# Optimization experiments

Measured on AMD Instinct MI355X. Metric: run time of the kernel, lower is better.

The kernel has to match this reference:

```python
import jax, jax.numpy as jnp
import numpy as np

NA = 100000  # number of a-type nodes (rows of adj)
NB = 100000  # number of b-type nodes (cols of adj)
NE = 1600000 # number of edges (nnz of adj)
BF = 128     # b_features
AF = 128     # a_features


def setup_inputs() -> dict:
    key = jax.random.key(0)
    k1, k2, k3, k4, k5, k6 = jax.random.split(key, 6)
    stdv = 1.0 / np.sqrt(BF)
    return {
        "b_input": jax.random.normal(k1, (NB, BF), dtype=jnp.float32),
        "edge_rows": jax.random.randint(k2, (NE,), 0, NA, dtype=jnp.int32),
        "edge_cols": jax.random.randint(k3, (NE,), 0, NB, dtype=jnp.int32),
        "edge_vals": jax.random.uniform(k4, (NE,), dtype=jnp.float32),
        "a_weight": jax.random.uniform(k5, (BF, AF), minval=-stdv, maxval=stdv, dtype=jnp.float32),
        "a_bias": jax.random.uniform(k6, (AF,), minval=-stdv, maxval=stdv, dtype=jnp.float32),
    }


def reference(b_input, edge_rows, edge_cols, edge_vals, a_weight, a_bias):
    # a_support = b_input @ a_weight            : [NB, AF]
    a_support = jnp.matmul(b_input, a_weight)
    # a_output = spmm(adj, a_support)           : [NA, AF]
    # adj[r, c] = edge_vals at (edge_rows, edge_cols)
    gathered = a_support[edge_cols] * edge_vals[:, None]   # [NE, AF]
    a_output = jax.ops.segment_sum(gathered, edge_rows, num_segments=NA)
    # bias=True -> early return of a-side output
    return a_output + a_bias
```

## Files before the change

kernel.cpp:

```cpp
#include <hip/hip_runtime.h>
#include <hip/hip_bf16.h>

#define AF 128
#define BF 128
#define BROWS 64
#define CAP 1600
#define PASSA_CHUNK 8192
#define NBUCK_MAX 1600

typedef __attribute__((ext_vector_type(8))) short bf16x8;
typedef __attribute__((ext_vector_type(4))) float f32x4;

__device__ inline unsigned short f2bf(float f) {
    unsigned int u = __float_as_uint(f);
    u += 0x7FFF + ((u >> 16) & 1);
    return (unsigned short)(u >> 16);
}
__device__ inline unsigned int pk2bf(float x, float y) {
    __hip_bfloat162 h = __float22bfloat162_rn(make_float2(x, y));
    return *(unsigned int*)&h;
}
__device__ inline float bflo(unsigned int u) { return __uint_as_float(u << 16); }
__device__ inline float bfhi(unsigned int u) { return __uint_as_float(u & 0xFFFF0000u); }

__global__ void wtrans_kernel(const float* __restrict__ W, unsigned short* __restrict__ Wt) {
    int idx = blockIdx.x * 256 + threadIdx.x;
    int n = idx & 127, k = idx >> 7;
    Wt[n * 128 + k] = f2bf(W[(size_t)k * 128 + n]);
}

__global__ __launch_bounds__(256) void gemm_mfma_kernel(const float* __restrict__ Bin,
                                                        const unsigned short* __restrict__ Wt,
                                                        unsigned short* __restrict__ Sup, int NB) {
    __shared__ unsigned short As[64][136];
    __shared__ unsigned short Ws[128][136];
    const int tid = threadIdx.x;
    const int lane = tid & 63;
    const int wave = tid >> 6;
    const int row0 = blockIdx.x * 64;

    {
        int lr = tid >> 2;
        int ks = (tid & 3) * 32;
        int gr = row0 + lr;
        const float4* src = (const float4*)(Bin + (size_t)gr * BF + ks);
        #pragma unroll
        for (int i = 0; i < 4; i++) {
            float4 a = (gr < NB) ? src[2 * i]     : make_float4(0.f, 0.f, 0.f, 0.f);
            float4 b = (gr < NB) ? src[2 * i + 1] : make_float4(0.f, 0.f, 0.f, 0.f);
            uint4 u;
            u.x = pk2bf(a.x, a.y); u.y = pk2bf(a.z, a.w);
            u.z = pk2bf(b.x, b.y); u.w = pk2bf(b.z, b.w);
            *(uint4*)(&As[lr][ks + i * 8]) = u;
        }
    }
    {
        int r = tid >> 1;
        int c = (tid & 1) * 64;
        const uint4* src = (const uint4*)(Wt + r * 128 + c);
        uint4* dst = (uint4*)(&Ws[r][c]);
        #pragma unroll
        for (int i = 0; i < 8; i++) dst[i] = src[i];
    }
    __syncthreads();

    const int m = lane & 15;
    const int quad = lane >> 4;

    bf16x8 af[4];
    #pragma unroll
    for (int ks = 0; ks < 4; ks++)
        af[ks] = *(const bf16x8*)(&As[wave * 16 + m][ks * 32 + quad * 8]);

    #pragma unroll
    for (int nt = 0; nt < 8; nt++) {
        f32x4 acc = {0.f, 0.f, 0.f, 0.f};
        #pragma unroll
        for (int ks = 0; ks < 4; ks++) {
            bf16x8 bf = *(const bf16x8*)(&Ws[nt * 16 + m][ks * 32 + quad * 8]);
            acc = __builtin_amdgcn_mfma_f32_16x16x32_bf16(af[ks], bf, acc, 0, 0, 0);
        }
        int f = nt * 16 + m;
        int si = ((f & 63) << 1) | (f >> 6);
        #pragma unroll
        for (int r = 0; r < 4; r++) {
            int row = row0 + wave * 16 + quad * 4 + r;
            if (row < NB) Sup[(size_t)row * AF + si] = f2bf(acc[r]);
        }
    }
}

__global__ __launch_bounds__(256) void passA_kernel(const int* __restrict__ rows,
                                                    const int* __restrict__ cols,
                                                    const float* __restrict__ vals,
                                                    int* __restrict__ grel,
                                                    int2* __restrict__ binned, int NE, int NBUCK) {
    __shared__ int h[NBUCK_MAX];
    __shared__ int rbase[NBUCK_MAX];
    int tid = threadIdx.x;
    for (int i = tid; i < NBUCK; i += 256) h[i] = 0;
    __syncthreads();
    int base = blockIdx.x * PASSA_CHUNK;
    #pragma unroll
    for (int i = 0; i < PASSA_CHUNK / 256; i++) {
        int e = base + tid + i * 256;
        if (e < NE) atomicAdd(&h[rows[e] >> 6], 1);
    }
    __syncthreads();
    for (int k = tid; k < NBUCK; k += 256) {
        int c = h[k];
        rbase[k] = k * CAP + (c ? atomicAdd(&grel[k], c) : 0);
        h[k] = 0;
    }
    __syncthreads();
    #pragma unroll
    for (int i = 0; i < PASSA_CHUNK / 256; i++) {
        int e = base + tid + i * 256;
        if (e < NE) {
            int r = rows[e];
            int k = r >> 6;
            int lp = atomicAdd(&h[k], 1);
            int2 p;
            p.x = cols[e] | ((r & 63) << 17);
            p.y = __float_as_int(vals[e]);
            binned[rbase[k] + lp] = p;
        }
    }
}

__global__ __launch_bounds__(512) void spmm_sorted_kernel(const unsigned short* __restrict__ Sup,
                                                          const int2* __restrict__ binned,
                                                          const int* __restrict__ grel,
                                                          const float* __restrict__ bias,
                                                          float* __restrict__ out, int NA) {
    __shared__ int   spx[CAP];
    __shared__ float spy[CAP];
    __shared__ int cnt[BROWS];
    __shared__ int sc[BROWS];
    __shared__ int rs[BROWS + 1];
    __shared__ int cur[BROWS];
    const int tid = threadIdx.x;
    const int b = blockIdx.x;
    int n = grel[b]; if (n > CAP) n = CAP;
    const int2* src = binned + (size_t)b * CAP;

    int2 pr[4];
    #pragma unroll
    for (int j = 0; j < 4; j++) {
        int i = tid + j * 512;
        pr[j] = (i < n) ? src[i] : make_int2(-1, 0);
    }
    if (tid < BROWS) cnt[tid] = 0;
    __syncthreads();
    #pragma unroll
    for (int j = 0; j < 4; j++)
        if (pr[j].x >= 0) atomicAdd(&cnt[(pr[j].x >> 17) & 63], 1);
    __syncthreads();
    int v = (tid < BROWS) ? cnt[tid] : 0;
    int x = v;
    if (tid < BROWS) sc[tid] = x;
    __syncthreads();
    #pragma unroll
    for (int off = 1; off < BROWS; off <<= 1) {
        int t = (tid < BROWS && tid >= off) ? sc[tid - off] : 0;
        __syncthreads();
        if (tid < BROWS) { x += t; sc[tid] = x; }
        __syncthreads();
    }
    if (tid < BROWS) { rs[tid] = x - v; cur[tid] = x - v; }
    if (tid == BROWS - 1) rs[BROWS] = x;
    __syncthreads();
    #pragma unroll
    for (int j = 0; j < 4; j++) {
        if (pr[j].x >= 0) {
            int lr = (pr[j].x >> 17) & 63;
            int pos = atomicAdd(&cur[lr], 1);
            spx[pos] = pr[j].x & 0x1FFFF;
            spy[pos] = __int_as_float(pr[j].y);
        }
    }
    __syncthreads();

    const int lane = tid & 63;
    const int wv = tid >> 6;
    const float b0 = bias[lane];
    const float b1 = bias[64 + lane];
    for (int lr = wv; lr < BROWS; lr += 8) {
        int row = b * BROWS + lr;
        if (row >= NA) break;
        int e = rs[lr], end = rs[lr + 1];
        float ax = 0.f, ay = 0.f;
        for (; e + 8 <= end; e += 8) {
            int c0 = spx[e],     c1 = spx[e + 1], c2 = spx[e + 2], c3 = spx[e + 3];
            int c4 = spx[e + 4], c5 = spx[e + 5], c6 = spx[e + 6], c7 = spx[e + 7];
            float v0 = spy[e],     v1 = spy[e + 1], v2 = spy[e + 2], v3 = spy[e + 3];
            float v4 = spy[e + 4], v5 = spy[e + 5], v6 = spy[e + 6], v7 = spy[e + 7];
            unsigned int s0 = *(const unsigned int*)(Sup + (size_t)c0 * AF + lane * 2);
            unsigned int s1 = *(const unsigned int*)(Sup + (size_t)c1 * AF + lane * 2);
            unsigned int s2 = *(const unsigned int*)(Sup + (size_t)c2 * AF + lane * 2);
            unsigned int s3 = *(const unsigned int*)(Sup + (size_t)c3 * AF + lane * 2);
            unsigned int s4 = *(const unsigned int*)(Sup + (size_t)c4 * AF + lane * 2);
            unsigned int s5 = *(const unsigned int*)(Sup + (size_t)c5 * AF + lane * 2);
            unsigned int s6 = *(const unsigned int*)(Sup + (size_t)c6 * AF + lane * 2);
            unsigned int s7 = *(const unsigned int*)(Sup + (size_t)c7 * AF + lane * 2);
            ax += v0 * bflo(s0) + v1 * bflo(s1) + v2 * bflo(s2) + v3 * bflo(s3)
                + v4 * bflo(s4) + v5 * bflo(s5) + v6 * bflo(s6) + v7 * bflo(s7);
            ay += v0 * bfhi(s0) + v1 * bfhi(s1) + v2 * bfhi(s2) + v3 * bfhi(s3)
                + v4 * bfhi(s4) + v5 * bfhi(s5) + v6 * bfhi(s6) + v7 * bfhi(s7);
        }
        for (; e < end; e++) {
            int c = spx[e];
            float vv = spy[e];
            unsigned int s = *(const unsigned int*)(Sup + (size_t)c * AF + lane * 2);
            ax += vv * bflo(s);
            ay += vv * bfhi(s);
        }
        out[(size_t)row * AF + lane]      = ax + b0;
        out[(size_t)row * AF + 64 + lane] = ay + b1;
    }
}

extern "C" void kernel_launch(void* const* d_in, const int* in_sizes, int n_in,
                              void* d_out, int out_size, void* d_ws, size_t ws_size,
                              hipStream_t stream) {
    const float* b_input   = (const float*)d_in[0];
    const int*   edge_rows = (const int*)d_in[1];
    const int*   edge_cols = (const int*)d_in[2];
    const float* edge_vals = (const float*)d_in[3];
    const float* a_weight  = (const float*)d_in[4];
    const float* a_bias    = (const float*)d_in[5];
    const int NB = in_sizes[0] / BF;
    const int NE = in_sizes[1];
    const int NA = out_size / AF;
    const int NBUCK = (NA + BROWS - 1) / BROWS;
    float* out = (float*)d_out;

    char* ws = (char*)d_ws;
    size_t off = 0;
    unsigned short* Sup = (unsigned short*)(ws + off); off += (size_t)NB * AF * sizeof(unsigned short);
    unsigned short* Wt  = (unsigned short*)(ws + off); off += (size_t)BF * AF * sizeof(unsigned short);
    int* grel = (int*)(ws + off); off += 2048 * sizeof(int);
    int2* binned = (int2*)(ws + off); off += (size_t)NBUCK * CAP * sizeof(int2);
    (void)ws_size; (void)n_in;

    hipMemsetAsync(grel, 0, 2048 * sizeof(int), stream);

    wtrans_kernel<<<64, 256, 0, stream>>>(a_weight, Wt);
    gemm_mfma_kernel<<<(NB + 63) / 64, 256, 0, stream>>>(b_input, Wt, Sup, NB);
    passA_kernel<<<(NE + PASSA_CHUNK - 1) / PASSA_CHUNK, 256, 0, stream>>>(
        edge_rows, edge_cols, edge_vals, grel, binned, NE, NBUCK);
    spmm_sorted_kernel<<<NBUCK, 512, 0, stream>>>(Sup, binned, grel, a_bias, out, NA);
}
```

Measured before the change: 260.4 us.

## Split edge binning into two-level coarse then fine bucketing passes

```diff
diff --git a/kernel.cpp b/kernel.cpp
--- a/kernel.cpp
+++ b/kernel.cpp
@@ -4,9 +4,11 @@
 #define AF 128
 #define BF 128
 #define BROWS 64
-#define CAP 1600
-#define PASSA_CHUNK 8192
-#define NBUCK_MAX 1600
+#define CAP_F 1600
+#define CROWS 1024
+#define CAP_C 18432
+#define CHUNK1 2048
+#define NCOARSE_MAX 128
 
 typedef __attribute__((ext_vector_type(8))) short bf16x8;
 typedef __attribute__((ext_vector_type(4))) float f32x4;
@@ -90,41 +92,77 @@
     }
 }
 
-__global__ __launch_bounds__(256) void passA_kernel(const int* __restrict__ rows,
-                                                    const int* __restrict__ cols,
-                                                    const float* __restrict__ vals,
-                                                    int* __restrict__ grel,
-                                                    int2* __restrict__ binned, int NE, int NBUCK) {
-    __shared__ int h[NBUCK_MAX];
-    __shared__ int rbase[NBUCK_MAX];
+__global__ __launch_bounds__(256) void passA1_kernel(const int* __restrict__ rows,
+                                                     const int* __restrict__ cols,
+                                                     const float* __restrict__ vals,
+                                                     int* __restrict__ grelC,
+                                                     int2* __restrict__ binnedC, int NE, int NCOARSE) {
+    __shared__ int h[NCOARSE_MAX];
+    __shared__ int rbase[NCOARSE_MAX];
     int tid = threadIdx.x;
-    for (int i = tid; i < NBUCK; i += 256) h[i] = 0;
-    __syncthreads();
-    int base = blockIdx.x * PASSA_CHUNK;
-    #pragma unroll
-    for (int i = 0; i < PASSA_CHUNK / 256; i++) {
+    if (tid < NCOARSE) h[tid] = 0;
+    __syncthreads();
+    int base = blockIdx.x * CHUNK1;
+    #pragma unroll
+    for (int i = 0; i < CHUNK1 / 256; i++) {
         int e = base + tid + i * 256;
-        if (e < NE) atomicAdd(&h[rows[e] >> 6], 1);
-    }
-    __syncthreads();
-    for (int k = tid; k < NBUCK; k += 256) {
-        int c = h[k];
-        rbase[k] = k * CAP + (c ? atomicAdd(&grel[k], c) : 0);
-        h[k] = 0;
-    }
-    __syncthreads();
-    #pragma unroll
-    for (int i = 0; i < PASSA_CHUNK / 256; i++) {
+        if (e < NE) atomicAdd(&h[rows[e] >> 10], 1);
+    }
+    __syncthreads();
+    if (tid < NCOARSE) {
+        int c = h[tid];
+        rbase[tid] = tid * CAP_C + (c ? atomicAdd(&grelC[tid], c) : 0);
+        h[tid] = 0;
+    }
+    __syncthreads();
+    #pragma unroll
+    for (int i = 0; i < CHUNK1 / 256; i++) {
         int e = base + tid + i * 256;
         if (e < NE) {
             int r = rows[e];
-            int k = r >> 6;
+            int k = r >> 10;
             int lp = atomicAdd(&h[k], 1);
             int2 p;
-            p.x = cols[e] | ((r & 63) << 17);
+            p.x = cols[e] | ((r & 1023) << 17);
             p.y = __float_as_int(vals[e]);
-            binned[rbase[k] + lp] = p;
-        }
+            binnedC[rbase[k] + lp] = p;
+        }
+    }
+}
+
+__global__ __launch_bounds__(256) void passA2_kernel(const int2* __restrict__ binnedC,
+                                                     const int* __restrict__ grelC,
+                                                     int* __restrict__ grelF,
+                                                     int2* __restrict__ binnedF, int NBUCK) {
+    __shared__ int h[16];
+    __shared__ int rb[16];
+    const int tid = threadIdx.x;
+    const int j = blockIdx.x >> 3;
+    const int s = blockIdx.x & 7;
+    int n = grelC[j]; if (n > CAP_C) n = CAP_C;
+    const int st = (n * s) >> 3;
+    const int en = (n * (s + 1)) >> 3;
+    const int2* src = binnedC + (size_t)j * CAP_C;
+    if (tid < 16) h[tid] = 0;
+    __syncthreads();
+    for (int i = st + tid; i < en; i += 256)
+        atomicAdd(&h[src[i].x >> 23], 1);
+    __syncthreads();
+    if (tid < 16) {
+        int c = h[tid];
+        int fine = j * 16 + tid;
+        rb[tid] = (fine < NBUCK) ? (fine * CAP_F + (c ? atomicAdd(&grelF[fine], c) : 0)) : 0;
+        h[tid] = 0;
+    }
+    __syncthreads();
+    for (int i = st + tid; i < en; i += 256) {
+        int2 p = src[i];
+        int sub = p.x >> 23;
+        int lp = atomicAdd(&h[sub], 1);
+        int2 q;
+        q.x = p.x & 0x7FFFFF;
+        q.y = p.y;
+        binnedF[(size_t)rb[sub] + lp] = q;
     }
 }
 
@@ -133,16 +171,16 @@
                                                           const int* __restrict__ grel,
                                                           const float* __restrict__ bias,
                                                           float* __restrict__ out, int NA) {
-    __shared__ int   spx[CAP];
-    __shared__ float spy[CAP];
+    __shared__ int   spx[CAP_F];
+    __shared__ float spy[CAP_F];
     __shared__ int cnt[BROWS];
     __shared__ int sc[BROWS];
     __shared__ int rs[BROWS + 1];
     __shared__ int cur[BROWS];
     const int tid = threadIdx.x;
     const int b = blockIdx.x;
-    int n = grel[b]; if (n > CAP) n = CAP;
-    const int2* src = binned + (size_t)b * CAP;
+    int n = grel[b]; if (n > CAP_F) n = CAP_F;
+    const int2* src = binned + (size_t)b * CAP_F;
 
     int2 pr[4];
     #pragma unroll
@@ -233,21 +271,25 @@
     const int NE = in_sizes[1];
     const int NA = out_size / AF;
     const int NBUCK = (NA + BROWS - 1) / BROWS;
+    const int NCOARSE = (NA + CROWS - 1) / CROWS;
     float* out = (float*)d_out;
 
     char* ws = (char*)d_ws;
     size_t off = 0;
     unsigned short* Sup = (unsigned short*)(ws + off); off += (size_t)NB * AF * sizeof(unsigned short);
     unsigned short* Wt  = (unsigned short*)(ws + off); off += (size_t)BF * AF * sizeof(unsigned short);
-    int* grel = (int*)(ws + off); off += 2048 * sizeof(int);
-    int2* binned = (int2*)(ws + off); off += (size_t)NBUCK * CAP * sizeof(int2);
+    int* grelC = (int*)(ws + off); off += 1024 * sizeof(int);
+    int* grelF = (int*)(ws + off); off += 2048 * sizeof(int);
+    int2* binnedC = (int2*)(ws + off); off += (size_t)NCOARSE * CAP_C * sizeof(int2);
+    int2* binnedF = (int2*)(ws + off); off += (size_t)NBUCK * CAP_F * sizeof(int2);
     (void)ws_size; (void)n_in;
 
-    hipMemsetAsync(grel, 0, 2048 * sizeof(int), stream);
+    hipMemsetAsync(grelC, 0, 3072 * sizeof(int), stream);
 
     wtrans_kernel<<<64, 256, 0, stream>>>(a_weight, Wt);
     gemm_mfma_kernel<<<(NB + 63) / 64, 256, 0, stream>>>(b_input, Wt, Sup, NB);
-    passA_kernel<<<(NE + PASSA_CHUNK - 1) / PASSA_CHUNK, 256, 0, stream>>>(
-        edge_rows, edge_cols, edge_vals, grel, binned, NE, NBUCK);
-    spmm_sorted_kernel<<<NBUCK, 512, 0, stream>>>(Sup, binned, grel, a_bias, out, NA);
-}
+    passA1_kernel<<<(NE + CHUNK1 - 1) / CHUNK1, 256, 0, stream>>>(
+        edge_rows, edge_cols, edge_vals, grelC, binnedC, NE, NCOARSE);
+    passA2_kernel<<<NCOARSE * 8, 256, 0, stream>>>(binnedC, grelC, grelF, binnedF, NBUCK);
+    spmm_sorted_kernel<<<NBUCK, 512, 0, stream>>>(Sup, binnedF, grelF, a_bias, out, NA);
+}
```

New measurement: 241.7 us. -7.2%, faster.
